# Kernel tuning notes

Hardware: AMD Instinct MI355X
Metric: run time of the kernel (lower is better)

## Reference

```python
import jax, jax.numpy as jnp
import numpy as np

EPS = 1e-6

def _l2norm(x, axis=-1):
    # F.normalize: x / max(||x||, eps) with eps=1e-12
    n = jnp.linalg.norm(x, axis=axis, keepdims=True)
    return x / jnp.maximum(n, 1e-12)

def setup_inputs() -> dict:
    key = jax.random.key(0)
    k1, k2, k3, k4, k5 = jax.random.split(key, 5)
    B, Na, Np, D, K = 16, 2048, 2048, 512, 32
    return {
        "anchor": jax.random.normal(k1, (B, Na, D), dtype=jnp.float32),
        "positive1": jax.random.normal(k2, (B, Np, D), dtype=jnp.float32),
        "positive2": jax.random.normal(k3, (B, Np, D), dtype=jnp.float32),
        "idx_a": jax.random.randint(k4, (B, K), 0, Na),
        "idx_p": jax.random.randint(k5, (B, K), 0, Na),
    }

def _match(a, p):
    # a: (B,Na,D), p: (B,Np,D) both unit-norm
    sim = jnp.einsum('bnd,bmd->bnm', a, p)          # (B,Na,Np) cosine sims
    idx = jnp.argmax(sim, axis=-1)                   # (B,Na) top-1 NN
    w = jnp.max(sim, axis=-1)                        # = gather(sim, idx)
    matched = jnp.take_along_axis(p, idx[..., None], axis=1)  # (B,Na,D)
    return matched, w

def reference(anchor, positive1, positive2, idx_a, idx_p):
    a = _l2norm(anchor)
    p1 = _l2norm(positive1)
    p2 = _l2norm(positive2)
    m1, w1 = _match(a, p1)
    m2, w2 = _match(a, p2)
    w1 = w1[..., None]
    w2 = w2[..., None]
    fused = (w1 * m1 + w2 * m2) / (w1 + w2 + EPS)    # (B,Na,D)
    fused = _l2norm(fused)
    A_s = jnp.take_along_axis(a, idx_a[..., None], axis=1)      # (B,K,D)
    P_s = jnp.take_along_axis(fused, idx_p[..., None], axis=1)  # (B,K,D)
    return (A_s, P_s)
```

## Files before the change

kernel.cpp:

```cpp
#include <hip/hip_runtime.h>

#define BB   16
#define NA   2048
#define NP   2048
#define DD   512
#define KSEL 32
#define TR   256
#define NT   (NP/TR)
#define DC   32
#define NCH  (DD/DC)

#define QT_OFF   0
#define QT_SZ    (BB*DD*KSEL)
#define PMAX_OFF (QT_OFF + QT_SZ)
#define PRED_SZ  (BB*2*NT*KSEL)
#define PIDX_OFF (PMAX_OFF + PRED_SZ)

__device__ __forceinline__ void gload_lds16(const void* g, void* l) {
  __builtin_amdgcn_global_load_lds(
      (const __attribute__((address_space(1))) unsigned int*)g,
      (__attribute__((address_space(3))) unsigned int*)l,
      16, 0, 0);
}

__global__ __launch_bounds__(256) void prep_kernel(
    const float* __restrict__ anchor, const int* __restrict__ idx_a,
    const int* __restrict__ idx_p, float* __restrict__ outA,
    float* __restrict__ qt_ws) {
  const int blk = blockIdx.x;
  const int b = blk >> 5, k = blk & 31;
  const int t = threadIdx.x;
  const int ia = idx_a[blk];
  const int ip = idx_p[blk];
  const float* rowA = anchor + ((size_t)(b*NA + ia))*DD;
  const float* rowP = anchor + ((size_t)(b*NA + ip))*DD;

  float2 a2 = *(const float2*)(rowA + 2*t);
  float2 p2 = *(const float2*)(rowP + 2*t);
  float sa = a2.x*a2.x + a2.y*a2.y;
  float sp = p2.x*p2.x + p2.y*p2.y;
  #pragma unroll
  for (int o = 1; o < 64; o <<= 1) {
    sa += __shfl_xor(sa, o, 64);
    sp += __shfl_xor(sp, o, 64);
  }
  __shared__ float lb[8];
  const int w = t >> 6, l = t & 63;
  if (l == 0) { lb[w] = sa; lb[4+w] = sp; }
  __syncthreads();
  sa = lb[0]+lb[1]+lb[2]+lb[3];
  sp = lb[4]+lb[5]+lb[6]+lb[7];
  const float ra = 1.f / fmaxf(sqrtf(sa), 1e-12f);
  const float rp = 1.f / fmaxf(sqrtf(sp), 1e-12f);

  float2 o2; o2.x = a2.x*ra; o2.y = a2.y*ra;
  *(float2*)(outA + (size_t)blk*DD + 2*t) = o2;

  const int d = 2*t;
  qt_ws[((size_t)b*DD + d  )*KSEL + k] = p2.x*rp;
  qt_ws[((size_t)b*DD + d+1)*KSEL + k] = p2.y*rp;
}

__global__ __launch_bounds__(256) void match_kernel(
    const float* __restrict__ p1, const float* __restrict__ p2,
    const float* __restrict__ qt_ws, float* __restrict__ pmax_ws,
    int* __restrict__ pidx_ws) {
  __shared__ float Qt[DD*KSEL];
  __shared__ float Ps[2][TR*DC];

  const int tile = blockIdx.x, mat = blockIdx.y, b = blockIdx.z;
  const float* __restrict__ P =
      (mat ? p2 : p1) + (size_t)b*NP*DD + (size_t)tile*TR*DD;
  const int t = threadIdx.x;
  const int w = t >> 6, l = t & 63;
  const int qg = t & 3;
  const int rg = t >> 2;

  {
    const float* src = qt_ws + (size_t)b*DD*KSEL;
    #pragma unroll
    for (int i = 0; i < 16; ++i) {
      const int idx4 = i*256 + t;
      *(float4*)&Qt[idx4*4] = *(const float4*)&src[idx4*4];
    }
  }

  {
    float* buf = &Ps[0][0];
    #pragma unroll
    for (int j = 0; j < 8; ++j) {
      const int r = w*64 + j*8 + (l >> 3);
      const int src_dc = (l & 7) ^ ((r >> 2) & 7);
      const float* g = P + (size_t)r*DD + 0*DC + src_dc*4;
      gload_lds16(g, buf + w*2048 + j*256);
    }
  }
  asm volatile("s_waitcnt vmcnt(0)" ::: "memory");
  __syncthreads();

  float acc[8][4];
  float ssq[4];
  #pragma unroll
  for (int jj = 0; jj < 8; ++jj)
    #pragma unroll
    for (int i = 0; i < 4; ++i) acc[jj][i] = 0.f;
  #pragma unroll
  for (int i = 0; i < 4; ++i) ssq[i] = 0.f;

  for (int c = 0; c < NCH; ++c) {
    const int cur = c & 1;
    if (c + 1 < NCH) {
      float* buf = &Ps[cur ^ 1][0];
      #pragma unroll
      for (int j = 0; j < 8; ++j) {
        const int r = w*64 + j*8 + (l >> 3);
        const int src_dc = (l & 7) ^ ((r >> 2) & 7);
        const float* g = P + (size_t)r*DD + (size_t)(c+1)*DC + src_dc*4;
        gload_lds16(g, buf + w*2048 + j*256);
      }
    }
    const float* __restrict__ pb = &Ps[cur][0];
    #pragma unroll
    for (int dc4 = 0; dc4 < 8; ++dc4) {
      float pr[4][4];
      #pragma unroll
      for (int i = 0; i < 4; ++i) {
        const int r = rg*4 + i;
        const int pc = dc4 ^ (rg & 7);
        const float4 v = *(const float4*)&pb[r*DC + pc*4];
        pr[i][0] = v.x; pr[i][1] = v.y; pr[i][2] = v.z; pr[i][3] = v.w;
      }
      #pragma unroll
      for (int kk = 0; kk < 4; ++kk) {
        const int dk = c*DC + dc4*4 + kk;
        const float4 q0 = *(const float4*)&Qt[dk*KSEL + qg*8];
        const float4 q1 = *(const float4*)&Qt[dk*KSEL + qg*8 + 4];
        #pragma unroll
        for (int i = 0; i < 4; ++i) {
          const float p = pr[i][kk];
          acc[0][i] += q0.x*p; acc[1][i] += q0.y*p;
          acc[2][i] += q0.z*p; acc[3][i] += q0.w*p;
          acc[4][i] += q1.x*p; acc[5][i] += q1.y*p;
          acc[6][i] += q1.z*p; acc[7][i] += q1.w*p;
          ssq[i] += p*p;
        }
      }
    }
    asm volatile("s_waitcnt vmcnt(0)" ::: "memory");
    __syncthreads();
  }

  float rinvp[4];
  #pragma unroll
  for (int i = 0; i < 4; ++i)
    rinvp[i] = 1.f / fmaxf(sqrtf(ssq[i]), 1e-12f);

  float* redv  = &Ps[0][0];
  int*   redi  = (int*)&Ps[0][2048];
  float* red2v = &Ps[0][4096];
  int*   red2i = (int*)&Ps[0][4096 + 256];

  #pragma unroll
  for (int jj = 0; jj < 8; ++jj) {
    const int q = qg*8 + jj;
    float best = -1e30f; int bi = 0;
    #pragma unroll
    for (int i = 0; i < 4; ++i) {
      const float s = acc[jj][i] * rinvp[i];
      if (s > best) { best = s; bi = rg*4 + i; }
    }
    redv[rg*32 + q] = best;
    redi[rg*32 + q] = bi;
  }
  __syncthreads();
  {
    const int g = t >> 5, q = t & 31;
    float best = -1e30f; int bi = 0;
    for (int rr = g*8; rr < g*8 + 8; ++rr) {
      const float v = redv[rr*32 + q];
      if (v > best) { best = v; bi = redi[rr*32 + q]; }
    }
    red2v[g*32 + q] = best;
    red2i[g*32 + q] = bi;
  }
  __syncthreads();
  if (t < 32) {
    const int q = t;
    float best = -1e30f; int bi = 0;
    for (int g = 0; g < 8; ++g) {
      const float v = red2v[g*32 + q];
      if (v > best) { best = v; bi = red2i[g*32 + q]; }
    }
    const int o = ((b*2 + mat)*NT + tile)*KSEL + q;
    pmax_ws[o] = best;
    pidx_ws[o] = tile*TR + bi;
  }
}

__global__ __launch_bounds__(256) void fuse_kernel(
    const float* __restrict__ p1, const float* __restrict__ p2,
    const float* __restrict__ pmax_ws, const int* __restrict__ pidx_ws,
    float* __restrict__ outP) {
  const int blk = blockIdx.x;
  const int b = blk >> 5, k = blk & 31;
  const int t = threadIdx.x;

  float w1 = -1e30f, w2 = -1e30f; int i1 = 0, i2 = 0;
  for (int tl = 0; tl < NT; ++tl) {
    const int o1 = ((b*2 + 0)*NT + tl)*KSEL + k;
    const float v = pmax_ws[o1];
    if (v > w1) { w1 = v; i1 = pidx_ws[o1]; }
    const int o2 = ((b*2 + 1)*NT + tl)*KSEL + k;
    const float u = pmax_ws[o2];
    if (u > w2) { w2 = u; i2 = pidx_ws[o2]; }
  }

  const float* r1 = p1 + ((size_t)b*NP + i1)*DD;
  const float* r2 = p2 + ((size_t)b*NP + i2)*DD;
  float2 a  = *(const float2*)(r1 + 2*t);
  float2 c2 = *(const float2*)(r2 + 2*t);
  float s1 = a.x*a.x + a.y*a.y;
  float s2 = c2.x*c2.x + c2.y*c2.y;
  #pragma unroll
  for (int o = 1; o < 64; o <<= 1) {
    s1 += __shfl_xor(s1, o, 64);
    s2 += __shfl_xor(s2, o, 64);
  }
  __shared__ float lb[12];
  const int w = t >> 6, l = t & 63;
  if (l == 0) { lb[w] = s1; lb[4+w] = s2; }
  __syncthreads();
  s1 = lb[0]+lb[1]+lb[2]+lb[3];
  s2 = lb[4]+lb[5]+lb[6]+lb[7];
  const float rn1 = 1.f / fmaxf(sqrtf(s1), 1e-12f);
  const float rn2 = 1.f / fmaxf(sqrtf(s2), 1e-12f);

  const float invd = 1.f / (w1 + w2 + 1e-6f);
  const float fx = (w1*(a.x*rn1)  + w2*(c2.x*rn2)) * invd;
  const float fy = (w1*(a.y*rn1)  + w2*(c2.y*rn2)) * invd;

  float sf = fx*fx + fy*fy;
  #pragma unroll
  for (int o = 1; o < 64; o <<= 1) sf += __shfl_xor(sf, o, 64);
  if (l == 0) lb[8+w] = sf;
  __syncthreads();
  sf = lb[8]+lb[9]+lb[10]+lb[11];
  const float rf = 1.f / fmaxf(sqrtf(sf), 1e-12f);

  float2 o2; o2.x = fx*rf; o2.y = fy*rf;
  *(float2*)(outP + (size_t)blk*DD + 2*t) = o2;
}

extern "C" void kernel_launch(void* const* d_in, const int* in_sizes, int n_in,
                              void* d_out, int out_size, void* d_ws, size_t ws_size,
                              hipStream_t stream) {
  (void)in_sizes; (void)n_in; (void)out_size; (void)ws_size;
  const float* anchor = (const float*)d_in[0];
  const float* p1     = (const float*)d_in[1];
  const float* p2     = (const float*)d_in[2];
  const int*   idx_a  = (const int*)d_in[3];
  const int*   idx_p  = (const int*)d_in[4];

  float* out  = (float*)d_out;
  float* outA = out;
  float* outP = out + (size_t)BB*KSEL*DD;

  float* ws   = (float*)d_ws;
  float* qt   = ws + QT_OFF;
  float* pmax = ws + PMAX_OFF;
  int*   pidx = (int*)(ws + PIDX_OFF);

  hipLaunchKernelGGL(prep_kernel, dim3(BB*KSEL), dim3(256), 0, stream,
                     anchor, idx_a, idx_p, outA, qt);
  hipLaunchKernelGGL(match_kernel, dim3(NT, 2, BB), dim3(256), 0, stream,
                     p1, p2, qt, pmax, pidx);
  hipLaunchKernelGGL(fuse_kernel, dim3(BB*KSEL), dim3(256), 0, stream,
                     p1, p2, pmax, pidx, outP);
}
```

Before: 212.9 us.

## Shrink match tiles to 64 rows, stream Q chunks via LDS, split D across lanes

The row tile per block in the match kernel drops from 256 to 64, so the grid grows fourfold. Instead of staging the whole 64 KB query matrix in LDS, each block now double-buffers 32-row chunks of Q with async global-to-LDS loads. This shrinks LDS use and allows four blocks per CU. Each group of four lanes splits the D dimension, partial dot products are combined with cross-lane shuffles, and the argmax reduction is simplified to one LDS pass. The cost is that each P tile is reused less per Q load, and the fuse kernel must scan four times as many partial maxima.

```diff
diff --git a/kernel.cpp b/kernel.cpp
--- a/kernel.cpp
+++ b/kernel.cpp
@@ -5,7 +5,7 @@
 #define NP   2048
 #define DD   512
 #define KSEL 32
-#define TR   256
+#define TR   64
 #define NT   (NP/TR)
 #define DC   32
 #define NCH  (DD/DC)
@@ -61,39 +61,56 @@
   qt_ws[((size_t)b*DD + d+1)*KSEL + k] = p2.y*rp;
 }
 
-__global__ __launch_bounds__(256) void match_kernel(
+__global__ __launch_bounds__(256, 4) void match_kernel(
     const float* __restrict__ p1, const float* __restrict__ p2,
     const float* __restrict__ qt_ws, float* __restrict__ pmax_ws,
     int* __restrict__ pidx_ws) {
-  __shared__ float Qt[DD*KSEL];
+  __shared__ float Qc[2][DC*KSEL];
   __shared__ float Ps[2][TR*DC];
 
   const int tile = blockIdx.x, mat = blockIdx.y, b = blockIdx.z;
   const float* __restrict__ P =
       (mat ? p2 : p1) + (size_t)b*NP*DD + (size_t)tile*TR*DD;
+  const float* __restrict__ Qsrc = qt_ws + (size_t)b*DD*KSEL;
   const int t = threadIdx.x;
   const int w = t >> 6, l = t & 63;
-  const int qg = t & 3;
-  const int rg = t >> 2;
-
+  const int qg  = l & 3;
+  const int ds  = (l >> 2) & 3;
+  const int rgl = l >> 4;
+  const int rg  = w*4 + rgl;
+
+  int p_srcoff[2];
+  #pragma unroll
+  for (int j = 0; j < 2; ++j) {
+    const int sid = j*256 + t;
+    const int r = sid >> 3, s = sid & 7;
+    const int dsd = ((s >> 1) ^ ((r >> 2) & 3)) & 3;
+    const int dhd = (s & 1) ^ ((r >> 2) & 1);
+    p_srcoff[j] = r*DD + dsd*8 + dhd*4;
+  }
+  int q_srcoff;
   {
-    const float* src = qt_ws + (size_t)b*DD*KSEL;
-    #pragma unroll
-    for (int i = 0; i < 16; ++i) {
-      const int idx4 = i*256 + t;
-      *(float4*)&Qt[idx4*4] = *(const float4*)&src[idx4*4];
-    }
-  }
+    const int dloc = t >> 3, s = t & 7;
+    const int dsd = dloc >> 3;
+    const int qgd = ((s >> 1) ^ dsd) & 3;
+    const int qhd = (s & 1) ^ (dsd & 1);
+    q_srcoff = dloc*KSEL + qgd*8 + qhd*4;
+  }
+
+  const int pc2 = ((ds ^ rgl) & 3) * 2;
+  const int pQ0 = pc2 + ((rgl & 1));
+  const int pQ1 = pc2 + (1 ^ (rgl & 1));
+  const int pRowBase = (w*16 + rgl*4) * DC;
+  const int qc2 = ((qg ^ ds) & 3) * 2;
+  const int qQ0 = qc2 + ((ds & 1));
+  const int qQ1 = qc2 + (1 ^ (ds & 1));
+  const int qRowBase = ds*8*KSEL;
 
   {
-    float* buf = &Ps[0][0];
-    #pragma unroll
-    for (int j = 0; j < 8; ++j) {
-      const int r = w*64 + j*8 + (l >> 3);
-      const int src_dc = (l & 7) ^ ((r >> 2) & 7);
-      const float* g = P + (size_t)r*DD + 0*DC + src_dc*4;
-      gload_lds16(g, buf + w*2048 + j*256);
-    }
+    float* pb = &Ps[0][0];
+    gload_lds16(P + p_srcoff[0],           pb + t*4);
+    gload_lds16(P + p_srcoff[1],           pb + (256 + t)*4);
+    gload_lds16(Qsrc + q_srcoff,           &Qc[0][0] + t*4);
   }
   asm volatile("s_waitcnt vmcnt(0)" ::: "memory");
   __syncthreads();
@@ -107,37 +124,34 @@
   #pragma unroll
   for (int i = 0; i < 4; ++i) ssq[i] = 0.f;
 
+  #pragma unroll 2
   for (int c = 0; c < NCH; ++c) {
     const int cur = c & 1;
     if (c + 1 < NCH) {
-      float* buf = &Ps[cur ^ 1][0];
+      float* pb = &Ps[cur ^ 1][0];
+      const int gc = (c + 1) * DC;
+      gload_lds16(P + (size_t)gc + p_srcoff[0], pb + t*4);
+      gload_lds16(P + (size_t)gc + p_srcoff[1], pb + (256 + t)*4);
+      gload_lds16(Qsrc + (size_t)gc*KSEL + q_srcoff, &Qc[cur ^ 1][0] + t*4);
+    }
+    const float* __restrict__ pb = &Ps[cur][0];
+    const float* __restrict__ qb = &Qc[cur][0];
+    #pragma unroll
+    for (int dh = 0; dh < 2; ++dh) {
+      const int pQ = dh ? pQ1 : pQ0;
+      float4 p4[4];
       #pragma unroll
-      for (int j = 0; j < 8; ++j) {
-        const int r = w*64 + j*8 + (l >> 3);
-        const int src_dc = (l & 7) ^ ((r >> 2) & 7);
-        const float* g = P + (size_t)r*DD + (size_t)(c+1)*DC + src_dc*4;
-        gload_lds16(g, buf + w*2048 + j*256);
-      }
-    }
-    const float* __restrict__ pb = &Ps[cur][0];
-    #pragma unroll
-    for (int dc4 = 0; dc4 < 8; ++dc4) {
-      float pr[4][4];
+      for (int i = 0; i < 4; ++i)
+        p4[i] = *(const float4*)&pb[pRowBase + i*DC + pQ*4];
       #pragma unroll
-      for (int i = 0; i < 4; ++i) {
-        const int r = rg*4 + i;
-        const int pc = dc4 ^ (rg & 7);
-        const float4 v = *(const float4*)&pb[r*DC + pc*4];
-        pr[i][0] = v.x; pr[i][1] = v.y; pr[i][2] = v.z; pr[i][3] = v.w;
-      }
-      #pragma unroll
-      for (int kk = 0; kk < 4; ++kk) {
-        const int dk = c*DC + dc4*4 + kk;
-        const float4 q0 = *(const float4*)&Qt[dk*KSEL + qg*8];
-        const float4 q1 = *(const float4*)&Qt[dk*KSEL + qg*8 + 4];
+      for (int dd2 = 0; dd2 < 4; ++dd2) {
+        const int drow = qRowBase + (dh*4 + dd2)*KSEL;
+        const float4 q0 = *(const float4*)&qb[drow + qQ0*4];
+        const float4 q1 = *(const float4*)&qb[drow + qQ1*4];
         #pragma unroll
         for (int i = 0; i < 4; ++i) {
-          const float p = pr[i][kk];
+          const float p = (dd2 == 0) ? p4[i].x : (dd2 == 1) ? p4[i].y
+                         : (dd2 == 2) ? p4[i].z : p4[i].w;
           acc[0][i] += q0.x*p; acc[1][i] += q0.y*p;
           acc[2][i] += q0.z*p; acc[3][i] += q0.w*p;
           acc[4][i] += q1.x*p; acc[5][i] += q1.y*p;
@@ -150,46 +164,49 @@
     __syncthreads();
   }
 
+  #pragma unroll
+  for (int jj = 0; jj < 8; ++jj)
+    #pragma unroll
+    for (int i = 0; i < 4; ++i) {
+      acc[jj][i] += __shfl_xor(acc[jj][i], 4, 64);
+      acc[jj][i] += __shfl_xor(acc[jj][i], 8, 64);
+    }
+  #pragma unroll
+  for (int i = 0; i < 4; ++i) {
+    ssq[i] += __shfl_xor(ssq[i], 4, 64);
+    ssq[i] += __shfl_xor(ssq[i], 8, 64);
+  }
+
   float rinvp[4];
   #pragma unroll
   for (int i = 0; i < 4; ++i)
     rinvp[i] = 1.f / fmaxf(sqrtf(ssq[i]), 1e-12f);
 
-  float* redv  = &Ps[0][0];
-  int*   redi  = (int*)&Ps[0][2048];
-  float* red2v = &Ps[0][4096];
-  int*   red2i = (int*)&Ps[0][4096 + 256];
-
-  #pragma unroll
-  for (int jj = 0; jj < 8; ++jj) {
-    const int q = qg*8 + jj;
-    float best = -1e30f; int bi = 0;
-    #pragma unroll
-    for (int i = 0; i < 4; ++i) {
-      const float s = acc[jj][i] * rinvp[i];
-      if (s > best) { best = s; bi = rg*4 + i; }
-    }
-    redv[rg*32 + q] = best;
-    redi[rg*32 + q] = bi;
-  }
-  __syncthreads();
-  {
-    const int g = t >> 5, q = t & 31;
-    float best = -1e30f; int bi = 0;
-    for (int rr = g*8; rr < g*8 + 8; ++rr) {
-      const float v = redv[rr*32 + q];
-      if (v > best) { best = v; bi = redi[rr*32 + q]; }
-    }
-    red2v[g*32 + q] = best;
-    red2i[g*32 + q] = bi;
+  float* redv = &Ps[0][0];
+  int*   redi = (int*)&Ps[0][512];
+
+  if (ds == 0) {
+    #pragma unroll
+    for (int jj = 0; jj < 8; ++jj) {
+      const int q = qg*8 + jj;
+      float best = -1e30f; int bi = 0;
+      #pragma unroll
+      for (int i = 0; i < 4; ++i) {
+        const float s = acc[jj][i] * rinvp[i];
+        if (s > best) { best = s; bi = rg*4 + i; }
+      }
+      redv[rg*32 + q] = best;
+      redi[rg*32 + q] = bi;
+    }
   }
   __syncthreads();
   if (t < 32) {
     const int q = t;
     float best = -1e30f; int bi = 0;
-    for (int g = 0; g < 8; ++g) {
-      const float v = red2v[g*32 + q];
-      if (v > best) { best = v; bi = red2i[g*32 + q]; }
+    #pragma unroll
+    for (int g = 0; g < 16; ++g) {
+      const float v = redv[g*32 + q];
+      if (v > best) { best = v; bi = redi[g*32 + q]; }
     }
     const int o = ((b*2 + mat)*NT + tile)*KSEL + q;
     pmax_ws[o] = best;
```

After: 318.7 us. 49.7% more time.
